# Kernel optimization log

Measured on AMD Instinct MI355X. Metric: run time of the kernel, lower is better.

The kernel has to match this reference:

```python
import jax, jax.numpy as jnp
import numpy as np

N, E, Z, C, B, G, T = 10000, 160000, 10, 64, 8, 16, 2
R_MAX = 5.0
AVG_NEIGH = 16.0
L_SLICES = ((0, 1), (1, 4), (4, 9))  # l=0,1,2 blocks of the 9 SH components


def sph_harm(u):
    # component-normalized real spherical harmonics up to l=2, u: [E,3] unit vectors
    x, y, z = u[:, 0], u[:, 1], u[:, 2]
    s3, s5, s15 = 3.0 ** 0.5, 5.0 ** 0.5, 15.0 ** 0.5
    return jnp.stack([
        jnp.ones_like(x),
        s3 * x, s3 * y, s3 * z,
        s15 * x * y, s15 * y * z, (s5 / 2) * (3 * z * z - 1), s15 * x * z, (s15 / 2) * (x * x - y * y),
    ], axis=1)  # [E,9]


def radial_embed(r):
    # Bessel basis * polynomial cutoff (p=5), r: [E]
    u = r / R_MAX
    n = jnp.arange(1, B + 1, dtype=jnp.float32)
    bessel = jnp.sqrt(2.0 / R_MAX) * jnp.sin(n[None, :] * jnp.pi * u[:, None]) / (r[:, None] + 1e-9)
    p = 5.0
    fc = 1 - (p + 1) * (p + 2) / 2 * u ** p + p * (p + 2) * u ** (p + 1) - p * (p + 1) / 2 * u ** (p + 2)
    fc = jnp.where(u < 1.0, fc, 0.0)
    return bessel * fc[:, None]  # [E,B]


def per_l_linear(x, W):
    # x: [n,C,9], W: [3,C,C]; independent channel mixing per l-block
    return jnp.concatenate([
        jnp.einsum('ncm,cd->ndm', x[:, :, s:e], W[l]) for l, (s, e) in enumerate(L_SLICES)
    ], axis=2)


def _forward(positions, node_attrs, charges, shifts, W_emb, atomic_energies,
             W_r1, W_r2, W_mix, W_sc, w_poly, W_prod, w_e, w_d,
             edge_index, batch, num_graphs):
    sender, receiver = edge_index[0], edge_index[1]
    # atomic reference energies
    node_e0 = node_attrs @ atomic_energies  # [N]
    e0 = jax.ops.segment_sum(node_e0, batch, num_segments=num_graphs)
    # node embedding: scalars only
    node_feats = jnp.zeros((positions.shape[0], C, 9), positions.dtype)
    node_feats = node_feats.at[:, :, 0].set(node_attrs @ W_emb)
    # edge geometry
    vec = positions[sender] - positions[receiver] + shifts  # [E,3]
    lengths = jnp.sqrt(jnp.sum(vec * vec, axis=1) + 1e-12)
    sh = sph_harm(vec / lengths[:, None])        # [E,9]
    edge_feats = radial_embed(lengths)           # [E,B]
    energies = [e0]
    dipoles = []
    for t in range(T):
        # radial MLP -> per-channel TP weights
        w = jax.nn.silu(edge_feats @ W_r1[t]) @ W_r2[t]      # [E,C]
        h_s = node_feats[sender, :, 0]                       # gather sender scalars [E,C]
        m = (w * h_s)[:, :, None] * sh[:, None, :]           # TP message [E,C,9]
        agg = jax.ops.segment_sum(m, receiver, num_segments=positions.shape[0]) / AVG_NEIGH
        msg = per_l_linear(agg, W_mix[t])
        sc = per_l_linear(node_feats, W_sc[t])               # self-connection
        # product basis (correlation 3): channel-wise scalar polynomial gate
        s0 = msg[:, :, 0]
        poly = w_poly[t, :, 0][None] + w_poly[t, :, 1][None] * s0 + w_poly[t, :, 2][None] * s0 * s0
        node_feats = per_l_linear(msg * poly[:, :, None], W_prod[t]) + sc
        # readout: 1x0e energy + 1x1o dipole
        e_n = node_feats[:, :, 0] @ w_e[t]                   # [N]
        energies.append(jax.ops.segment_sum(e_n, batch, num_segments=num_graphs))
        dipoles.append(jnp.einsum('ncm,c->nm', node_feats[:, :, 1:4], w_d[t]))  # [N,3]
    contributions = jnp.stack(energies, axis=-1)             # [G,T+1]
    total_energy = jnp.sum(contributions, axis=-1)           # [G]
    atomic_dipoles = jnp.sum(jnp.stack(dipoles, axis=-1), axis=-1)  # [N,3]
    total_dipole = jax.ops.segment_sum(atomic_dipoles, batch, num_segments=num_graphs)
    total_dipole = total_dipole + jax.ops.segment_sum(charges[:, None] * positions, batch, num_segments=num_graphs)
    return total_energy, contributions, atomic_dipoles, total_dipole


def setup_inputs():
    key = jax.random.key(0)
    ks = jax.random.split(key, 16)
    s = 0.1
    species = jax.random.randint(ks[1], (N,), 0, Z)
    return {
        'positions': jax.random.normal(ks[0], (N, 3)) * 3.0,
        'node_attrs': jax.nn.one_hot(species, Z, dtype=jnp.float32),
        'charges': jax.random.normal(ks[2], (N,)) * 0.1,
        'shifts': jnp.zeros((E, 3), jnp.float32),
        'W_emb': jax.random.normal(ks[5], (Z, C)) * s,
        'atomic_energies': jax.random.normal(ks[6], (Z,)) * s,
        'W_r1': jax.random.normal(ks[7], (T, B, 64)) * s,
        'W_r2': jax.random.normal(ks[8], (T, 64, C)) * s,
        'W_mix': jax.random.normal(ks[9], (T, 3, C, C)) * s,
        'W_sc': jax.random.normal(ks[10], (T, 3, C, C)) * s,
        'w_poly': jax.random.normal(ks[11], (T, C, 3)) * s,
        'W_prod': jax.random.normal(ks[12], (T, 3, C, C)) * s,
        'w_e': jax.random.normal(ks[13], (T, C)) * s,
        'w_d': jax.random.normal(ks[14], (T, C)) * s,
        'edge_index': jax.random.randint(ks[3], (2, E), 0, N),
        'batch': jnp.sort(jax.random.randint(ks[4], (N,), 0, G)),
        'num_graphs': G,
    }


def reference(positions, node_attrs, charges, shifts, W_emb, atomic_energies,
              W_r1, W_r2, W_mix, W_sc, w_poly, W_prod, w_e, w_d,
              edge_index, batch, num_graphs):
    args = (node_attrs, charges, shifts, W_emb, atomic_energies, W_r1, W_r2,
            W_mix, W_sc, w_poly, W_prod, w_e, w_d, edge_index, batch, num_graphs)
    total_energy, contributions, atomic_dipoles, total_dipole = _forward(positions, *args)
    forces = -jax.grad(lambda p: jnp.sum(_forward(p, *args)[0]))(positions)
    return total_energy, contributions, forces, total_dipole, atomic_dipoles
```

## Files before the change

kernel.cpp:

```cpp
#include <hip/hip_runtime.h>
#include <hip/hip_bf16.h>

#define NN 10000
#define NE 160000
#define NZ 10
#define NBES 8
#define NG 16
#define NT 2
#define NB 2048
#define NB1 2049
#define PL ((size_t)NN*64)

static constexpr float PI_F  = 3.14159265358979323846f;
static constexpr float KBES  = 0.63245553203367587f;
static constexpr float S3    = 1.73205080756887729f;

static constexpr size_t OFF_UVL  = 0;
static constexpr size_t OFF_PIN  = OFF_UVL + (size_t)NE*4;
static constexpr size_t OFF_ATT  = OFF_PIN + (size_t)NN*3;
static constexpr size_t OFF_CHG  = OFF_ATT + (size_t)NN*NZ;
static constexpr size_t OFF_SHF  = OFF_CHG + (size_t)NN;
static constexpr size_t OFF_NF0  = OFF_SHF + (size_t)NE*3;
static constexpr size_t OFF_NF1  = OFF_NF0 + PL;
static constexpr size_t OFF_MSG0 = OFF_NF1 + 4*PL;
static constexpr size_t OFF_MSG1 = OFF_MSG0 + 4*PL;
static constexpr size_t OFF_AGG  = OFF_MSG1 + 4*PL;
static constexpr size_t O_GA1    = OFF_AGG;
static constexpr size_t O_GA0    = OFF_AGG + 2*PL;
static constexpr size_t OFF_W    = OFF_AGG + 4*PL;
static constexpr size_t O_WEMB   = OFF_W;
static constexpr size_t O_AE     = O_WEMB + 640;
static constexpr size_t O_R1     = O_AE   + 16;
static constexpr size_t O_R2     = O_R1   + 1024;
static constexpr size_t O_WMIX   = O_R2   + 8192;
static constexpr size_t O_WMIXT  = O_WMIX + 24576;
static constexpr size_t O_WSC    = O_WMIXT+ 24576;
static constexpr size_t O_WSCT   = O_WSC  + 24576;
static constexpr size_t O_WPROD  = O_WSCT + 24576;
static constexpr size_t O_WPRODT = O_WPROD+ 24576;
static constexpr size_t O_WPOLY  = O_WPRODT+24576;
static constexpr size_t O_WE     = O_WPOLY+ 384;
static constexpr size_t O_WD     = O_WE   + 128;
static constexpr size_t OFF_ACC  = O_WD   + 128;
static constexpr size_t O_E0G    = OFF_ACC;
static constexpr size_t O_ETG    = O_E0G + 16;
static constexpr size_t O_TD     = O_ETG + 32;
static constexpr size_t O_ADP    = O_TD  + 48;
static constexpr size_t O_GPOS   = O_ADP + (size_t)NN*3;
static constexpr size_t ACC_FLOATS = 96 + (size_t)NN*6;
static constexpr size_t O_EN0    = O_GPOS + (size_t)NN*3;
static constexpr size_t O_EN1    = O_EN0 + NN;
static constexpr size_t O_E0N    = O_EN1 + NN;
static constexpr size_t O_FLAG   = O_E0N + NN;
static constexpr size_t O_TW     = O_FLAG + 4;
static constexpr size_t O_TQ     = O_TW + (size_t)2*NB1*64;
static constexpr size_t O_OFFR   = O_TQ + (size_t)2*NB1*64;
static constexpr size_t O_OFFS   = O_OFFR + (NN+1);
static constexpr size_t O_CURR   = O_OFFS + (NN+1);
static constexpr size_t O_CURS   = O_CURR + NN;
static constexpr size_t O_RECRAW = O_CURS + NN;
static constexpr size_t O_RECR   = (O_RECRAW + 7) & ~(size_t)7;
static constexpr size_t O_RECS   = O_RECR + (size_t)NE*8;
static constexpr size_t WS_FLOATS= O_RECS + (size_t)NE*8;

__device__ __forceinline__ float rlane(float v, int l){
  return __int_as_float(__builtin_amdgcn_readlane(__float_as_int(v), l));
}

static constexpr int LD_CNT[14] = {NN*3, NN*NZ, NN, NE*3, NZ*64, NZ, NT*NBES*64, NT*64*64,
                                   NT*3*64*64, NT*3*64*64, NT*64*3, NT*3*64*64, NT*64, NT*64};
static constexpr int LD_TOTAL = NN*3 + NN*NZ + NN + NE*3 + NZ*64 + NZ + NT*NBES*64 + NT*64*64
                              + 3*(NT*3*64*64) + NT*64*3 + 4*(NT*64) - NT*64*2;
__global__ __launch_bounds__(256) void k_load_all(
    const void* s0, const void* s1, const void* s2, const void* s3, const void* s4,
    const void* s5, const void* s6, const void* s7, const void* s8, const void* s9,
    const void* s10, const void* s11, const void* s12, const void* s13,
    float* __restrict__ ws){
  __shared__ int found;
  if (threadIdx.x == 0) found = 0;
  __syncthreads();
  const unsigned* raw = (const unsigned*)s1;
  int f = 0;
  for (int i = threadIdx.x; i < 4096; i += 256){
    unsigned w = raw[i];
    f |= (w == 0x00003F80u || w == 0x3F803F80u) ? 1 : 0;
  }
  if (f) found = 1;
  __syncthreads();
  const int isbf = found;
  if (blockIdx.x == 0 && threadIdx.x == 0) ((int*)(ws + O_FLAG))[0] = isbf;

  const void* srcs[14] = {s0,s1,s2,s3,s4,s5,s6,s7,s8,s9,s10,s11,s12,s13};
  const size_t dsts[14] = {OFF_PIN, OFF_ATT, OFF_CHG, OFF_SHF, O_WEMB, O_AE, O_R1, O_R2,
                           O_WMIX, O_WSC, O_WPOLY, O_WPROD, O_WE, O_WD};
  int i = blockIdx.x*256 + threadIdx.x;
  int seg = -1, off = i;
  #pragma unroll
  for (int j = 0; j < 14; ++j){
    if (seg < 0){
      if (off < LD_CNT[j]) seg = j;
      else off -= LD_CNT[j];
    }
  }
  if (seg < 0) return;
  float v = isbf ? __bfloat162float(((const __hip_bfloat16*)srcs[seg])[off])
                 : ((const float*)srcs[seg])[off];
  ws[dsts[seg] + off] = v;
}

__global__ void k_transpose_all(float* __restrict__ ws){
  const size_t srcs[3] = {O_WMIX, O_WSC, O_WPROD};
  const size_t dsts[3] = {O_WMIXT, O_WSCT, O_WPRODT};
  int i = blockIdx.x*256 + threadIdx.x;
  if (i >= 18*4096) return;
  int mm = i >> 12, r = (i >> 6) & 63, c = i & 63;
  int grp = mm / 6, m = mm % 6;
  ws[dsts[grp] + (size_t)m*4096 + (size_t)c*64 + r] =
      ws[srcs[grp] + (size_t)m*4096 + (size_t)r*64 + c];
}

static constexpr int GEOM_B = (NE+255)/256;
static constexpr int TAB_B  = (2*NB1+3)/4;
static constexpr int INIT_B = (NN+3)/4;
__global__ __launch_bounds__(256, 3) void k_prep(float* __restrict__ ws, const int* __restrict__ ei){
  int b = blockIdx.x;
  if (b < GEOM_B){
    int e = b*256 + threadIdx.x;
    if (e >= NE) return;
    const float* pos = ws + OFF_PIN;
    const float* shifts = ws + OFF_SHF;
    int s = ei[e], r = ei[NE + e];
    float vx = pos[s*3+0] - pos[r*3+0] + shifts[(size_t)e*3+0];
    float vy = pos[s*3+1] - pos[r*3+1] + shifts[(size_t)e*3+1];
    float vz = pos[s*3+2] - pos[r*3+2] + shifts[(size_t)e*3+2];
    float L = sqrtf(vx*vx + vy*vy + vz*vz + 1e-12f);
    float inv = 1.f / L;
    float4 uq; uq.x = vx*inv; uq.y = vy*inv; uq.z = vz*inv; uq.w = L;
    *(float4*)(ws + OFF_UVL + (size_t)e*4) = uq;
    if (L < 5.f){
      atomicAdd((int*)(ws + O_CURR) + r, 1);
      atomicAdd((int*)(ws + O_CURS) + s, 1);
    }
  } else if (b < GEOM_B + TAB_B){
    int lane = threadIdx.x & 63;
    int task = (b - GEOM_B)*4 + (threadIdx.x >> 6);
    if (task >= 2*NB1) return;
    int t = task / NB1, node = task % NB1;
    const float* R1 = ws + O_R1 + (size_t)t*512;
    const float* R2 = ws + O_R2 + (size_t)t*4096;
    float r1c[8];
    #pragma unroll
    for (int j = 0; j < 8; ++j) r1c[j] = R1[j*64 + lane];
    float L = fmaxf((float)node * (5.f/NB), 1e-6f);
    float ur = L*0.2f;
    float ef[8], dd[8];
    if (ur < 1.f){
      float u2=ur*ur, u4=u2*u2, u5=u4*ur;
      float fc = 1.f - 21.f*u5 + 35.f*u5*ur - 15.f*u5*u2;
      float omu = 1.f - ur;
      float dfc = -105.f*u4*omu*omu;
      float invr = 1.f/(L + 1e-9f);
      #pragma unroll
      for (int bb = 0; bb < 8; ++bb){
        float nb = (float)(bb+1);
        float arg = nb*PI_F*ur;
        float sn = __sinf(arg), cs = __cosf(arg);
        float bes = KBES*sn*invr;
        float dbes = KBES*(nb*PI_F*0.2f)*cs*invr - bes*invr;
        ef[bb] = bes*fc;
        dd[bb] = dbes*fc + bes*dfc*0.2f;
      }
    } else {
      #pragma unroll
      for (int bb = 0; bb < 8; ++bb){ ef[bb] = 0.f; dd[bb] = 0.f; }
    }
    float a = 0.f, tt = 0.f;
    #pragma unroll
    for (int bb = 0; bb < 8; ++bb){ a = fmaf(ef[bb], r1c[bb], a); tt = fmaf(r1c[bb], dd[bb], tt); }
    float sg = 1.f/(1.f + __expf(-a));
    float sl = a*sg;
    float q  = sg*fmaf(a, 1.f - sg, 1.f)*tt;
    float r2c[64];
    #pragma unroll
    for (int j = 0; j < 64; ++j) r2c[j] = R2[j*64 + lane];
    float W0=0.f, W1=0.f, Q0=0.f, Q1=0.f;
    #pragma unroll
    for (int j = 0; j < 64; j += 2){
      W0 = fmaf(rlane(sl, j  ), r2c[j  ], W0);
      W1 = fmaf(rlane(sl, j+1), r2c[j+1], W1);
      Q0 = fmaf(rlane(q,  j  ), r2c[j  ], Q0);
      Q1 = fmaf(rlane(q,  j+1), r2c[j+1], Q1);
    }
    size_t idx = ((size_t)t*NB1 + node)*64 + lane;
    ws[O_TW + idx] = (W0+W1)*(1.f/16.f);
    ws[O_TQ + idx] = (Q0+Q1)*(1.f/16.f);
  } else {
    int lane = threadIdx.x & 63;
    int n = (b - GEOM_B - TAB_B)*4 + (threadIdx.x >> 6);
    if (n >= NN) return;
    const float* attrs = ws + OFF_ATT;
    float acc = 0.f;
    #pragma unroll
    for (int z = 0; z < NZ; ++z) acc = fmaf(attrs[(size_t)n*NZ+z], ws[O_WEMB + z*64 + lane], acc);
    ws[OFF_NF0 + (size_t)n*64 + lane] = acc;
    if (lane == 0){
      float e = 0.f;
      #pragma unroll
      for (int z = 0; z < NZ; ++z) e = fmaf(attrs[(size_t)n*NZ+z], ws[O_AE + z], e);
      ws[O_E0N + n] = e;
    }
  }
}

__global__ __launch_bounds__(1024) void k_csr_scan(
    int* __restrict__ curr, int* __restrict__ curs,
    int* __restrict__ offr, int* __restrict__ offs_){
  __shared__ unsigned short cr[NN], cs[NN];
  __shared__ int pr[1024], ps[1024];
  int tid = threadIdx.x;
  for (int i = tid; i < NN; i += 1024){
    cr[i] = (unsigned short)curr[i];
    cs[i] = (unsigned short)curs[i];
  }
  __syncthreads();
  const int chunk = (NN + 1023)/1024;
  int lo = tid*chunk, hi = lo + chunk;
  if (hi > NN) hi = NN;
  if (lo > NN) lo = NN;
  int sr = 0, ss = 0;
  for (int i = lo; i < hi; ++i){ sr += cr[i]; ss += cs[i]; }
  pr[tid] = sr; ps[tid] = ss;
  __syncthreads();
  for (int o = 1; o < 1024; o <<= 1){
    int vr = (tid >= o) ? pr[tid-o] : 0;
    int vs = (tid >= o) ? ps[tid-o] : 0;
    __syncthreads();
    pr[tid] += vr; ps[tid] += vs;
    __syncthreads();
  }
  int runr = tid ? pr[tid-1] : 0;
  int runs = tid ? ps[tid-1] : 0;
  for (int i = lo; i < hi; ++i){
    int a = cr[i], c = cs[i];
    offr[i] = runr; curr[i] = runr; runr += a;
    offs_[i] = runs; curs[i] = runs; runs += c;
  }
  if (tid == 1023){ offr[NN] = runr; offs_[NN] = runs; }
}

__global__ void k_csr_fill(const int* __restrict__ ei, const float* __restrict__ uvl,
                           int* __restrict__ curr, int* __restrict__ curs,
                           float* __restrict__ recr, float* __restrict__ recs){
  int e = blockIdx.x*256 + threadIdx.x;
  if (e >= NE) return;
  float4 q = *(const float4*)(uvl + (size_t)e*4);
  if (q.w >= 5.f) return;
  int s = ei[e], r = ei[NE + e];
  int4 meta; meta.x = s; meta.y = r; meta.z = e; meta.w = 0;
  int pr = atomicAdd(&curr[r], 1);
  *(float4*)(recr + (size_t)pr*8) = q;
  *(int4*)(recr + (size_t)pr*8 + 4) = meta;
  int ps = atomicAdd(&curs[s], 1);
  *(float4*)(recs + (size_t)ps*8) = q;
  *(int4*)(recs + (size_t)ps*8 + 4) = meta;
}

__global__ __launch_bounds__(256) void k_agg(
    const float* __restrict__ TWt, const float* __restrict__ recr,
    const float* __restrict__ h, const int* __restrict__ offr,
    float* __restrict__ agg){
  int lane = threadIdx.x & 63;
  int wid = blockIdx.x*4 + (threadIdx.x >> 6);
  int nw  = gridDim.x*4;
  for (int n = wid; n < NN; n += nw){
    int lo = offr[n], hi = offr[n+1];
    float c0=0.f, x1=0.f, y1=0.f, z1=0.f;
    float d0=0.f, x2=0.f, y2=0.f, z2=0.f;
    int i = lo;
    for (; i+1 < hi; i += 2){
      const float4 qa = *(const float4*)(recr + (size_t)i*8);
      const int sa = __builtin_amdgcn_readfirstlane(((const int*)(recr + (size_t)i*8 + 4))[0]);
      const float4 qb = *(const float4*)(recr + (size_t)(i+1)*8);
      const int sb = __builtin_amdgcn_readfirstlane(((const int*)(recr + (size_t)(i+1)*8 + 4))[0]);
      float pa = qa.w*(NB/5.f); int ba = (int)pa; float fa = pa - (float)ba;
      float pb = qb.w*(NB/5.f); int bbq = (int)pb; float fb = pb - (float)bbq;
      const float* Ta = TWt + (size_t)ba*64 + lane;
      const float* Tb = TWt + (size_t)bbq*64 + lane;
      float ta0 = Ta[0], tb0 = Tb[0];
      float wa = fmaf(Ta[64]-ta0, fa, ta0);
      float wb = fmaf(Tb[64]-tb0, fb, tb0);
      float wha = wa * h[(size_t)sa*64 + lane];
      float whb = wb * h[(size_t)sb*64 + lane];
      c0 += wha; d0 += whb;
      x1 = fmaf(wha, qa.x, x1); x2 = fmaf(whb, qb.x, x2);
      y1 = fmaf(wha, qa.y, y1); y2 = fmaf(whb, qb.y, y2);
      z1 = fmaf(wha, qa.z, z1); z2 = fmaf(whb, qb.z, z2);
    }
    if (i < hi){
      const float4 q = *(const float4*)(recr + (size_t)i*8);
      const int sU = __builtin_amdgcn_readfirstlane(((const int*)(recr + (size_t)i*8 + 4))[0]);
      float pa = q.w*(NB/5.f); int ba = (int)pa; float fa = pa - (float)ba;
      const float* Ta = TWt + (size_t)ba*64 + lane;
      float ta0 = Ta[0];
      float wa = fmaf(Ta[64]-ta0, fa, ta0);
      float wha = wa * h[(size_t)sU*64 + lane];
      c0 += wha;
      x1 = fmaf(wha, q.x, x1);
      y1 = fmaf(wha, q.y, y1);
      z1 = fmaf(wha, q.z, z1);
    }
    size_t ob = (size_t)n*64 + lane;
    agg[ob]        = c0 + d0;
    agg[ob+PL]     = S3*(x1 + x2);
    agg[ob+2*PL]   = S3*(y1 + y2);
    agg[ob+3*PL]   = S3*(z1 + z2);
  }
}

__global__ __launch_bounds__(256, 3) void k_lin2(
    const float* __restrict__ in, const float* __restrict__ W3, float* __restrict__ out){
  int k = blockIdx.y;
  int l = (k==0) ? 0 : 1;
  const float* W = W3 + (size_t)l*4096;
  int lane = threadIdx.x & 63;
  float wcol[64];
  #pragma unroll
  for (int j = 0; j < 64; ++j) wcol[j] = W[j*64 + lane];
  int wid = blockIdx.x*4 + (threadIdx.x >> 6);
  int nw  = gridDim.x*4;
  const float* inp = in + (size_t)k*PL;
  float* outp = out + (size_t)k*PL;
  for (int n = wid; n < NN; n += nw){
    float x = inp[(size_t)n*64 + lane];
    float a0 = 0.f, a1 = 0.f, a2 = 0.f, a3 = 0.f;
    #pragma unroll
    for (int j = 0; j < 64; j += 4){
      a0 = fmaf(rlane(x, j  ), wcol[j  ], a0);
      a1 = fmaf(rlane(x, j+1), wcol[j+1], a1);
      a2 = fmaf(rlane(x, j+2), wcol[j+2], a2);
      a3 = fmaf(rlane(x, j+3), wcol[j+3], a3);
    }
    outp[(size_t)n*64 + lane] = (a0+a1) + (a2+a3);
  }
}

template<int WRITE_NF, int NF_SINGLE>
__global__ __launch_bounds__(256, 3) void k_tail(
    const float* __restrict__ nf_in, const float* __restrict__ msg,
    const float* __restrict__ Wsc, const float* __restrict__ Wprod, const float* __restrict__ wp,
    const float* __restrict__ we, const float* __restrict__ wd,
    float* __restrict__ nf_out, float* __restrict__ en, float* __restrict__ adp){
  int lane = threadIdx.x & 63;
  int k = threadIdx.x >> 6;
  int l = (k==0) ? 0 : 1;
  const bool use_sc = !(NF_SINGLE && k > 0);
  float wcs[64], wcp[64];
  #pragma unroll
  for (int j = 0; j < 64; ++j)
    wcp[j] = Wprod[(size_t)l*4096 + j*64 + lane];
  if (use_sc){
    #pragma unroll
    for (int j = 0; j < 64; ++j)
      wcs[j] = Wsc[(size_t)l*4096 + j*64 + lane];
  }
  float p0 = wp[lane*3], p1 = wp[lane*3+1], p2 = wp[lane*3+2];
  float rw = (k==0) ? we[lane] : wd[lane];
  const float* msgk = msg + (size_t)k*PL;
  const float* nfk  = nf_in + (size_t)k*PL;
  float* outk = nf_out + (size_t)k*PL;
  for (int n = blockIdx.x; n < NN; n += gridDim.x){
    size_t base = (size_t)n*64 + lane;
    float s0 = msg[base];
    float xm = (k==0) ? s0 : msgk[base];
    float xg = xm * fmaf(fmaf(p2, s0, p1), s0, p0);
    float b0=0.f, b1=0.f;
    #pragma unroll
    for (int j = 0; j < 64; j += 2){
      b0 = fmaf(rlane(xg, j  ), wcp[j  ], b0);
      b1 = fmaf(rlane(xg, j+1), wcp[j+1], b1);
    }
    float out = b0 + b1;
    if (use_sc){
      float xs = nfk[base];
      float a0=0.f, a1=0.f;
      #pragma unroll
      for (int j = 0; j < 64; j += 2){
        a0 = fmaf(rlane(xs, j  ), wcs[j  ], a0);
        a1 = fmaf(rlane(xs, j+1), wcs[j+1], a1);
      }
      out += a0 + a1;
    }
    if (WRITE_NF) outk[base] = out;
    float red = out * rw;
    #pragma unroll
    for (int o = 32; o; o >>= 1) red += __shfl_xor(red, o, 64);
    if (lane == 0){
      if (k == 0) en[n] = red;
      else        adp[n*3 + (k-1)] += red;
    }
  }
}

__global__ __launch_bounds__(256, 3) void k_gback1(
    const float* __restrict__ WPRODT1, const float* __restrict__ we1,
    const float* __restrict__ msg1, const float* __restrict__ wp,
    const float* __restrict__ WMIXT1, float* __restrict__ out){
  int lane = threadIdx.x & 63;
  float wcol[64];
  #pragma unroll
  for (int j = 0; j < 64; ++j) wcol[j] = WMIXT1[j*64 + lane];
  float g = 0.f;
  #pragma unroll
  for (int c = 0; c < 64; ++c) g = fmaf(we1[c], WPRODT1[c*64 + lane], g);
  float p0 = wp[lane*3], p1 = wp[lane*3+1], p2 = wp[lane*3+2];
  int wid = blockIdx.x*4 + (threadIdx.x >> 6);
  int nw  = gridDim.x*4;
  for (int n = wid; n < NN; n += nw){
    float s0 = msg1[(size_t)n*64 + lane];
    float poly = fmaf(fmaf(p2, s0, p1), s0, p0);
    float dp   = fmaf(2.f*p2, s0, p1);
    float gb = g*fmaf(s0, dp, poly);
    float a0=0.f, a1=0.f, a2=0.f, a3=0.f;
    #pragma unroll
    for (int j = 0; j < 64; j += 4){
      a0 = fmaf(rlane(gb, j  ), wcol[j  ], a0);
      a1 = fmaf(rlane(gb, j+1), wcol[j+1], a1);
      a2 = fmaf(rlane(gb, j+2), wcol[j+2], a2);
      a3 = fmaf(rlane(gb, j+3), wcol[j+3], a3);
    }
    out[(size_t)n*64 + lane] = (a0+a1) + (a2+a3);
  }
}

__global__ __launch_bounds__(256) void k_ghg0(float* __restrict__ ws, const int* __restrict__ offs_){
  __shared__ float wl[2*4096];
  for (int i = threadIdx.x; i < 4096; i += 256){
    wl[i]        = ws[O_WPRODT + i];
    wl[4096 + i] = ws[O_WMIXT + i];
  }
  __syncthreads();
  const int lane = threadIdx.x & 63;
  int wid = blockIdx.x*4 + (threadIdx.x >> 6);
  const int nw = gridDim.x*4;
  float gnfc = ws[O_WE + lane];
  {
    const float* WS1 = ws + O_WSCT + 12288;
    const float* we1 = ws + O_WE + 64;
    #pragma unroll
    for (int c = 0; c < 64; ++c) gnfc = fmaf(we1[c], WS1[c*64 + lane], gnfc);
  }
  const float p0 = ws[O_WPOLY + lane*3];
  const float p1 = ws[O_WPOLY + lane*3 + 1];
  const float p2 = ws[O_WPOLY + lane*3 + 2];
  const float* TW1 = ws + O_TW + (size_t)NB1*64;
  const float* recs = ws + O_RECS;
  const float* GA1 = ws + O_GA1;
  for (int n = wid; n < NN; n += nw){
    int lo = offs_[n], hi = offs_[n+1];
    float acc = 0.f, acc2 = 0.f;
    int i = lo;
    for (; i+1 < hi; i += 2){
      const float4 qa = *(const float4*)(recs + (size_t)i*8);
      const int ra = __builtin_amdgcn_readfirstlane(((const int*)(recs + (size_t)i*8 + 4))[1]);
      const float4 qb = *(const float4*)(recs + (size_t)(i+1)*8);
      const int rb = __builtin_amdgcn_readfirstlane(((const int*)(recs + (size_t)(i+1)*8 + 4))[1]);
      float pa = qa.w*(NB/5.f); int ba = (int)pa; float fa = pa - (float)ba;
      float pb = qb.w*(NB/5.f); int bbq = (int)pb; float fb = pb - (float)bbq;
      const float* Ta = TW1 + (size_t)ba*64 + lane;
      const float* Tb = TW1 + (size_t)bbq*64 + lane;
      float ta0 = Ta[0], tb0 = Tb[0];
      float wa = fmaf(Ta[64]-ta0, fa, ta0);
      float wb = fmaf(Tb[64]-tb0, fb, tb0);
      acc  = fmaf(wa, GA1[(size_t)ra*64 + lane], acc);
      acc2 = fmaf(wb, GA1[(size_t)rb*64 + lane], acc2);
    }
    if (i < hi){
      const float4 q = *(const float4*)(recs + (size_t)i*8);
      const int rU = __builtin_amdgcn_readfirstlane(((const int*)(recs + (size_t)i*8 + 4))[1]);
      float pa = q.w*(NB/5.f); int ba = (int)pa; float fa = pa - (float)ba;
      const float* Ta = TW1 + (size_t)ba*64 + lane;
      float ta0 = Ta[0];
      float wa = fmaf(Ta[64]-ta0, fa, ta0);
      acc = fmaf(wa, GA1[(size_t)rU*64 + lane], acc);
    }
    float gB = gnfc + (acc + acc2);
    float q0=0.f, q1=0.f;
    #pragma unroll
    for (int j = 0; j < 64; j += 2){
      q0 = fmaf(rlane(gB,j),   wl[j*64 + lane],     q0);
      q1 = fmaf(rlane(gB,j+1), wl[(j+1)*64 + lane], q1);
    }
    float gmp = q0 + q1;
    float s0v = ws[OFF_MSG0 + (size_t)n*64 + lane];
    float poly = fmaf(fmaf(p2, s0v, p1), s0v, p0);
    float dp   = fmaf(2.f*p2, s0v, p1);
    float gb = gmp * fmaf(s0v, dp, poly);
    float u0=0.f, u1=0.f;
    #pragma unroll
    for (int j = 0; j < 64; j += 2){
      u0 = fmaf(rlane(gb,j),   wl[4096 + j*64 + lane],     u0);
      u1 = fmaf(rlane(gb,j+1), wl[4096 + (j+1)*64 + lane], u1);
    }
    ws[O_GA0 + (size_t)n*64 + lane] = u0 + u1;
  }
}

__global__ __launch_bounds__(256) void k_bwdE2(float* __restrict__ ws, const int* __restrict__ nlive_ptr){
  const int lane = threadIdx.x & 63;
  int wid = blockIdx.x*4 + (threadIdx.x >> 6);
  const int nw = gridDim.x*4;
  const int nlive = nlive_ptr[0];
  const float* recs = ws + O_RECS;
  const float* TQ  = ws + O_TQ;
  const float* h0  = ws + OFF_NF0;
  const float* h1  = ws + OFF_NF1;
  const float* ga0 = ws + O_GA0;
  const float* ga1 = ws + O_GA1;
  float* gpos = ws + O_GPOS;
  for (int i = wid; i < nlive; i += nw){
    const float4 q = *(const float4*)(recs + (size_t)i*8);
    const int* meta = (const int*)(recs + (size_t)i*8 + 4);
    const int s = __builtin_amdgcn_readfirstlane(meta[0]);
    const int r = __builtin_amdgcn_readfirstlane(meta[1]);
    float posb = q.w*(NB/5.f);
    int bi = (int)posb;
    float fr = posb - (float)bi;
    const float* T0 = TQ + (size_t)bi*64 + lane;
    const float* T1 = T0 + (size_t)NB1*64;
    float Q0 = fmaf(T0[64]-T0[0], fr, T0[0]);
    float Q1 = fmaf(T1[64]-T1[0], fr, T1[0]);
    float rr = Q0*h0[(size_t)s*64 + lane]*ga0[(size_t)r*64 + lane]
             + Q1*h1[(size_t)s*64 + lane]*ga1[(size_t)r*64 + lane];
    #pragma unroll
    for (int o = 32; o; o >>= 1) rr += __shfl_xor(rr, o, 64);
    if (lane < 3){
      float u = (lane==0) ? q.x : ((lane==1) ? q.y : q.z);
      float v = rr*u;
      atomicAdd(&gpos[(size_t)s*3 + lane],  v);
      atomicAdd(&gpos[(size_t)r*3 + lane], -v);
    }
  }
}

__global__ void k_reduce(const float* __restrict__ e0n, const float* __restrict__ en0,
                         const float* __restrict__ en1, const float* __restrict__ adp,
                         const float* __restrict__ q, const float* __restrict__ pos,
                         const int* __restrict__ batch, float* __restrict__ e0g,
                         float* __restrict__ Etg, float* __restrict__ td){
  int n = blockIdx.x*256 + threadIdx.x;
  int lane = threadIdx.x & 63;
  bool valid = (n < NN);
  int g = valid ? batch[n] : -1;
  float v0=0.f, v1=0.f, v2=0.f, tx=0.f, ty=0.f, tz=0.f;
  if (valid){
    v0 = e0n[n]; v1 = en0[n]; v2 = en1[n];
    float qq = q[n];
    tx = adp[n*3+0] + qq*pos[n*3+0];
    ty = adp[n*3+1] + qq*pos[n*3+1];
    tz = adp[n*3+2] + qq*pos[n*3+2];
  }
  int g0 = __shfl(g, 0, 64), g63 = __shfl(g, 63, 64);
  if (g0 == g63 && g0 >= 0){
    #pragma unroll
    for (int o = 32; o; o >>= 1){
      v0 += __shfl_xor(v0, o, 64); v1 += __shfl_xor(v1, o, 64); v2 += __shfl_xor(v2, o, 64);
      tx += __shfl_xor(tx, o, 64); ty += __shfl_xor(ty, o, 64); tz += __shfl_xor(tz, o, 64);
    }
    if (lane == 0){
      atomicAdd(&e0g[g0], v0); atomicAdd(&Etg[g0], v1); atomicAdd(&Etg[16+g0], v2);
      atomicAdd(&td[g0*3+0], tx); atomicAdd(&td[g0*3+1], ty); atomicAdd(&td[g0*3+2], tz);
    }
  } else if (valid){
    atomicAdd(&e0g[g], v0); atomicAdd(&Etg[g], v1); atomicAdd(&Etg[16+g], v2);
    atomicAdd(&td[g*3+0], tx); atomicAdd(&td[g*3+1], ty); atomicAdd(&td[g*3+2], tz);
  }
}

__global__ void k_writeout(const float* __restrict__ e0g, const float* __restrict__ Etg,
                           const float* __restrict__ td, const float* __restrict__ adp,
                           const float* __restrict__ gpos, void* __restrict__ outv,
                           const int* __restrict__ flag){
  int i = blockIdx.x*256 + threadIdx.x;
  const int total = NG + NG*3 + NN*3 + NG*3 + NN*3;
  if (i >= total) return;
  float v;
  if (i < 16){
    v = e0g[i] + Etg[i] + Etg[16+i];
  } else if (i < 64){
    int j = i - 16; int g = j/3, t = j - g*3;
    v = (t == 0) ? e0g[g] : Etg[(t-1)*16 + g];
  } else if (i < 64 + NN*3){
    v = -gpos[i-64];
  } else if (i < 64 + NN*3 + 48){
    v = td[i - (64 + NN*3)];
  } else {
    v = adp[i - (64 + NN*3 + 48)];
  }
  if (flag[0]) ((__hip_bfloat16*)outv)[i] = __float2bfloat16(v);
  else         ((float*)outv)[i] = v;
}

extern "C" void kernel_launch(void* const* d_in, const int* in_sizes, int n_in,
                              void* d_out, int out_size, void* d_ws, size_t ws_size,
                              hipStream_t stream) {
  if (ws_size < WS_FLOATS*sizeof(float)) return;
  const int* ei    = (const int*)d_in[14];
  const int* batch = (const int*)d_in[15];
  float* ws = (float*)d_ws;

  int* offr  = (int*)(ws + O_OFFR);
  int* offs_ = (int*)(ws + O_OFFS);
  int* curr  = (int*)(ws + O_CURR);
  int* curs  = (int*)(ws + O_CURS);

  hipMemsetAsync(ws + OFF_ACC, 0, ACC_FLOATS*sizeof(float), stream);
  hipMemsetAsync(curr, 0, 2*NN*sizeof(int), stream);

  k_load_all<<<(LD_TOTAL+255)/256, 256, 0, stream>>>(
      d_in[0], d_in[1], d_in[2], d_in[3], d_in[4], d_in[5], d_in[6], d_in[7],
      d_in[8], d_in[9], d_in[10], d_in[11], d_in[12], d_in[13], ws);
  k_transpose_all<<<288, 256, 0, stream>>>(ws);
  k_prep<<<GEOM_B + TAB_B + INIT_B, 256, 0, stream>>>(ws, ei);
  k_csr_scan<<<1, 1024, 0, stream>>>(curr, curs, offr, offs_);
  k_csr_fill<<<(NE+255)/256, 256, 0, stream>>>(ei, ws+OFF_UVL, curr, curs,
                                               ws+O_RECR, ws+O_RECS);

  const size_t NF[2]  = {OFF_NF0, OFF_NF1};
  const size_t MSG[2] = {OFF_MSG0, OFF_MSG1};
  dim3 ling(256, 4);

  for (int t = 0; t < NT; ++t){
    k_agg<<<1024, 256, 0, stream>>>(ws+O_TW + (size_t)t*NB1*64, ws+O_RECR,
                                    ws+NF[t], offr, ws+OFF_AGG);
    k_lin2<<<ling, 256, 0, stream>>>(ws+OFF_AGG, ws+O_WMIX + (size_t)t*12288, ws+MSG[t]);
    if (t == 0){
      k_tail<1,1><<<1024, 256, 0, stream>>>(ws+NF[0], ws+MSG[0],
                                            ws+O_WSC, ws+O_WPROD,
                                            ws+O_WPOLY, ws+O_WE, ws+O_WD,
                                            ws+OFF_NF1, ws+O_EN0, ws+O_ADP);
    } else {
      k_tail<0,0><<<1024, 256, 0, stream>>>(ws+NF[1], ws+MSG[1],
                                            ws+O_WSC + 12288, ws+O_WPROD + 12288,
                                            ws+O_WPOLY + 192, ws+O_WE + 64, ws+O_WD + 64,
                                            ws+OFF_NF1, ws+O_EN1, ws+O_ADP);
    }
  }

  k_gback1<<<1024, 256, 0, stream>>>(ws+O_WPRODT+12288, ws+O_WE+64,
                                     ws+OFF_MSG1, ws+O_WPOLY+192,
                                     ws+O_WMIXT+12288, ws+O_GA1);
  k_ghg0<<<1024, 256, 0, stream>>>(ws, offs_);
  k_bwdE2<<<2048, 256, 0, stream>>>(ws, offs_ + NN);

  k_reduce<<<(NN+255)/256, 256, 0, stream>>>(ws+O_E0N, ws+O_EN0, ws+O_EN1, ws+O_ADP,
                                             ws+OFF_CHG, ws+OFF_PIN, batch,
                                             ws+O_E0G, ws+O_ETG, ws+O_TD);
  k_writeout<<<(60112+255)/256, 256, 0, stream>>>(ws+O_E0G, ws+O_ETG, ws+O_TD, ws+O_ADP,
                                                  ws+O_GPOS, d_out, (const int*)(ws+O_FLAG));
}
```

Baseline: 335.9 us.

## Fuse channel-mix linear into node tail kernel and fold small kernels into neighbors

Merges k_lin2 (per-l channel mixing) with k_tail into one k_node kernel per layer. The scalar message is shared across the four l-component warps through double-buffered shared memory, and only the scalar message is stored, which shrinks the message buffers. The weight transpose moves into extra blocks of k_prep and now covers only the needed matrices, and the per-graph reduction moves into extra blocks of k_ghg0, removing several launches and an intermediate round trip to global memory. In exchange each thread holds three 64-float weight columns, so occupancy is lower (launch bounds 2), the grid is smaller, and there is a block-wide sync per node.

```diff
diff --git a/kernel.cpp b/kernel.cpp
--- a/kernel.cpp
+++ b/kernel.cpp
@@ -23,8 +23,8 @@
 static constexpr size_t OFF_NF0  = OFF_SHF + (size_t)NE*3;
 static constexpr size_t OFF_NF1  = OFF_NF0 + PL;
 static constexpr size_t OFF_MSG0 = OFF_NF1 + 4*PL;
-static constexpr size_t OFF_MSG1 = OFF_MSG0 + 4*PL;
-static constexpr size_t OFF_AGG  = OFF_MSG1 + 4*PL;
+static constexpr size_t OFF_MSG1 = OFF_MSG0 + PL;
+static constexpr size_t OFF_AGG  = OFF_MSG1 + PL;
 static constexpr size_t O_GA1    = OFF_AGG;
 static constexpr size_t O_GA0    = OFF_AGG + 2*PL;
 static constexpr size_t OFF_W    = OFF_AGG + 4*PL;
@@ -108,20 +108,10 @@
   ws[dsts[seg] + off] = v;
 }
 
-__global__ void k_transpose_all(float* __restrict__ ws){
-  const size_t srcs[3] = {O_WMIX, O_WSC, O_WPROD};
-  const size_t dsts[3] = {O_WMIXT, O_WSCT, O_WPRODT};
-  int i = blockIdx.x*256 + threadIdx.x;
-  if (i >= 18*4096) return;
-  int mm = i >> 12, r = (i >> 6) & 63, c = i & 63;
-  int grp = mm / 6, m = mm % 6;
-  ws[dsts[grp] + (size_t)m*4096 + (size_t)c*64 + r] =
-      ws[srcs[grp] + (size_t)m*4096 + (size_t)r*64 + c];
-}
-
 static constexpr int GEOM_B = (NE+255)/256;
 static constexpr int TAB_B  = (2*NB1+3)/4;
 static constexpr int INIT_B = (NN+3)/4;
+static constexpr int TRAN_B = 5*4096/256;
 __global__ __launch_bounds__(256, 3) void k_prep(float* __restrict__ ws, const int* __restrict__ ei){
   int b = blockIdx.x;
   if (b < GEOM_B){
@@ -194,7 +184,7 @@
     size_t idx = ((size_t)t*NB1 + node)*64 + lane;
     ws[O_TW + idx] = (W0+W1)*(1.f/16.f);
     ws[O_TQ + idx] = (Q0+Q1)*(1.f/16.f);
-  } else {
+  } else if (b < GEOM_B + TAB_B + INIT_B){
     int lane = threadIdx.x & 63;
     int n = (b - GEOM_B - TAB_B)*4 + (threadIdx.x >> 6);
     if (n >= NN) return;
@@ -209,6 +199,12 @@
       for (int z = 0; z < NZ; ++z) e = fmaf(attrs[(size_t)n*NZ+z], ws[O_AE + z], e);
       ws[O_E0N + n] = e;
     }
+  } else {
+    int i = (b - GEOM_B - TAB_B - INIT_B)*256 + threadIdx.x;
+    int mat = i >> 12, r = (i >> 6) & 63, c = i & 63;
+    const size_t src[5] = {O_WMIX, O_WMIX+12288, O_WPROD, O_WPROD+12288, O_WSC+12288};
+    const size_t dst[5] = {O_WMIXT, O_WMIXT+12288, O_WPRODT, O_WPRODT+12288, O_WSCT+12288};
+    ws[dst[mat] + (size_t)c*64 + r] = ws[src[mat] + (size_t)r*64 + c];
   }
 }
 
@@ -317,62 +313,53 @@
   }
 }
 
-__global__ __launch_bounds__(256, 3) void k_lin2(
-    const float* __restrict__ in, const float* __restrict__ W3, float* __restrict__ out){
-  int k = blockIdx.y;
-  int l = (k==0) ? 0 : 1;
-  const float* W = W3 + (size_t)l*4096;
-  int lane = threadIdx.x & 63;
-  float wcol[64];
+static constexpr int NODE_GRID = 512;
+template<int TI>
+__global__ __launch_bounds__(256, 2) void k_node(float* __restrict__ ws){
+  __shared__ float s0buf[2][64];
+  const int lane = threadIdx.x & 63;
+  const int k = threadIdx.x >> 6;
+  const int l = (k==0) ? 0 : 1;
+  const float* Wm = ws + O_WMIX  + TI*12288 + (size_t)l*4096;
+  const float* Wp = ws + O_WPROD + TI*12288 + (size_t)l*4096;
+  const float* Wsc= ws + O_WSC   + TI*12288 + (size_t)l*4096;
+  const bool use_sc = (TI==1) || (k==0);
+  float wcm[64], wcp[64], wcs[64];
   #pragma unroll
-  for (int j = 0; j < 64; ++j) wcol[j] = W[j*64 + lane];
-  int wid = blockIdx.x*4 + (threadIdx.x >> 6);
-  int nw  = gridDim.x*4;
-  const float* inp = in + (size_t)k*PL;
-  float* outp = out + (size_t)k*PL;
-  for (int n = wid; n < NN; n += nw){
-    float x = inp[(size_t)n*64 + lane];
-    float a0 = 0.f, a1 = 0.f, a2 = 0.f, a3 = 0.f;
+  for (int j = 0; j < 64; ++j) wcm[j] = Wm[j*64 + lane];
+  #pragma unroll
+  for (int j = 0; j < 64; ++j) wcp[j] = Wp[j*64 + lane];
+  if (use_sc){
+    #pragma unroll
+    for (int j = 0; j < 64; ++j) wcs[j] = Wsc[j*64 + lane];
+  }
+  const float p0 = ws[O_WPOLY + TI*192 + lane*3];
+  const float p1 = ws[O_WPOLY + TI*192 + lane*3 + 1];
+  const float p2 = ws[O_WPOLY + TI*192 + lane*3 + 2];
+  const float rw = (k==0) ? ws[O_WE + TI*64 + lane] : ws[O_WD + TI*64 + lane];
+  const float* aggk = ws + OFF_AGG + (size_t)k*PL;
+  const float* nfk  = (TI==0) ? (ws + OFF_NF0) : (ws + OFF_NF1 + (size_t)k*PL);
+  float* msgp = ws + (TI==0 ? OFF_MSG0 : OFF_MSG1);
+  float* nfo  = ws + OFF_NF1 + (size_t)k*PL;
+  float* en   = ws + (TI==0 ? O_EN0 : O_EN1);
+  float* adp  = ws + O_ADP;
+  int it = 0;
+  for (int n = blockIdx.x; n < NN; n += NODE_GRID, ++it){
+    size_t base = (size_t)n*64 + lane;
+    float a = aggk[base];
+    float m0=0.f, m1=0.f, m2=0.f, m3=0.f;
     #pragma unroll
     for (int j = 0; j < 64; j += 4){
-      a0 = fmaf(rlane(x, j  ), wcol[j  ], a0);
-      a1 = fmaf(rlane(x, j+1), wcol[j+1], a1);
-      a2 = fmaf(rlane(x, j+2), wcol[j+2], a2);
-      a3 = fmaf(rlane(x, j+3), wcol[j+3], a3);
-    }
-    outp[(size_t)n*64 + lane] = (a0+a1) + (a2+a3);
-  }
-}
-
-template<int WRITE_NF, int NF_SINGLE>
-__global__ __launch_bounds__(256, 3) void k_tail(
-    const float* __restrict__ nf_in, const float* __restrict__ msg,
-    const float* __restrict__ Wsc, const float* __restrict__ Wprod, const float* __restrict__ wp,
-    const float* __restrict__ we, const float* __restrict__ wd,
-    float* __restrict__ nf_out, float* __restrict__ en, float* __restrict__ adp){
-  int lane = threadIdx.x & 63;
-  int k = threadIdx.x >> 6;
-  int l = (k==0) ? 0 : 1;
-  const bool use_sc = !(NF_SINGLE && k > 0);
-  float wcs[64], wcp[64];
-  #pragma unroll
-  for (int j = 0; j < 64; ++j)
-    wcp[j] = Wprod[(size_t)l*4096 + j*64 + lane];
-  if (use_sc){
-    #pragma unroll
-    for (int j = 0; j < 64; ++j)
-      wcs[j] = Wsc[(size_t)l*4096 + j*64 + lane];
-  }
-  float p0 = wp[lane*3], p1 = wp[lane*3+1], p2 = wp[lane*3+2];
-  float rw = (k==0) ? we[lane] : wd[lane];
-  const float* msgk = msg + (size_t)k*PL;
-  const float* nfk  = nf_in + (size_t)k*PL;
-  float* outk = nf_out + (size_t)k*PL;
-  for (int n = blockIdx.x; n < NN; n += gridDim.x){
-    size_t base = (size_t)n*64 + lane;
-    float s0 = msg[base];
-    float xm = (k==0) ? s0 : msgk[base];
-    float xg = xm * fmaf(fmaf(p2, s0, p1), s0, p0);
+      m0 = fmaf(rlane(a, j  ), wcm[j  ], m0);
+      m1 = fmaf(rlane(a, j+1), wcm[j+1], m1);
+      m2 = fmaf(rlane(a, j+2), wcm[j+2], m2);
+      m3 = fmaf(rlane(a, j+3), wcm[j+3], m3);
+    }
+    float m = (m0+m1) + (m2+m3);
+    if (k == 0) s0buf[it & 1][lane] = m;
+    __syncthreads();
+    float s0 = s0buf[it & 1][lane];
+    float xg = m * fmaf(fmaf(p2, s0, p1), s0, p0);
     float b0=0.f, b1=0.f;
     #pragma unroll
     for (int j = 0; j < 64; j += 2){
@@ -390,7 +377,8 @@
       }
       out += a0 + a1;
     }
-    if (WRITE_NF) outk[base] = out;
+    if (TI == 0) nfo[base] = out;
+    if (k == 0) msgp[base] = s0;
     float red = out * rw;
     #pragma unroll
     for (int o = 32; o; o >>= 1) red += __shfl_xor(red, o, 64);
@@ -432,8 +420,42 @@
   }
 }
 
-__global__ __launch_bounds__(256) void k_ghg0(float* __restrict__ ws, const int* __restrict__ offs_){
+static constexpr int GHG_GRID = 1024;
+static constexpr int RED_B = (NN+255)/256;
+__global__ __launch_bounds__(256) void k_ghg0(float* __restrict__ ws, const int* __restrict__ offs_,
+                                              const int* __restrict__ batch){
   __shared__ float wl[2*4096];
+  if (blockIdx.x >= GHG_GRID){
+    int n = (blockIdx.x - GHG_GRID)*256 + threadIdx.x;
+    int lane = threadIdx.x & 63;
+    bool valid = (n < NN);
+    int g = valid ? batch[n] : -1;
+    float v0=0.f, v1=0.f, v2=0.f, tx=0.f, ty=0.f, tz=0.f;
+    if (valid){
+      v0 = ws[O_E0N + n]; v1 = ws[O_EN0 + n]; v2 = ws[O_EN1 + n];
+      float qq = ws[OFF_CHG + n];
+      tx = ws[O_ADP + n*3+0] + qq*ws[OFF_PIN + n*3+0];
+      ty = ws[O_ADP + n*3+1] + qq*ws[OFF_PIN + n*3+1];
+      tz = ws[O_ADP + n*3+2] + qq*ws[OFF_PIN + n*3+2];
+    }
+    float* e0g = ws + O_E0G; float* Etg = ws + O_ETG; float* td = ws + O_TD;
+    int g0 = __shfl(g, 0, 64), g63 = __shfl(g, 63, 64);
+    if (g0 == g63 && g0 >= 0){
+      #pragma unroll
+      for (int o = 32; o; o >>= 1){
+        v0 += __shfl_xor(v0, o, 64); v1 += __shfl_xor(v1, o, 64); v2 += __shfl_xor(v2, o, 64);
+        tx += __shfl_xor(tx, o, 64); ty += __shfl_xor(ty, o, 64); tz += __shfl_xor(tz, o, 64);
+      }
+      if (lane == 0){
+        atomicAdd(&e0g[g0], v0); atomicAdd(&Etg[g0], v1); atomicAdd(&Etg[16+g0], v2);
+        atomicAdd(&td[g0*3+0], tx); atomicAdd(&td[g0*3+1], ty); atomicAdd(&td[g0*3+2], tz);
+      }
+    } else if (valid){
+      atomicAdd(&e0g[g], v0); atomicAdd(&Etg[g], v1); atomicAdd(&Etg[16+g], v2);
+      atomicAdd(&td[g*3+0], tx); atomicAdd(&td[g*3+1], ty); atomicAdd(&td[g*3+2], tz);
+    }
+    return;
+  }
   for (int i = threadIdx.x; i < 4096; i += 256){
     wl[i]        = ws[O_WPRODT + i];
     wl[4096 + i] = ws[O_WMIXT + i];
@@ -441,7 +463,7 @@
   __syncthreads();
   const int lane = threadIdx.x & 63;
   int wid = blockIdx.x*4 + (threadIdx.x >> 6);
-  const int nw = gridDim.x*4;
+  const int nw = GHG_GRID*4;
   float gnfc = ws[O_WE + lane];
   {
     const float* WS1 = ws + O_WSCT + 12288;
@@ -542,40 +564,6 @@
   }
 }
 
-__global__ void k_reduce(const float* __restrict__ e0n, const float* __restrict__ en0,
-                         const float* __restrict__ en1, const float* __restrict__ adp,
-                         const float* __restrict__ q, const float* __restrict__ pos,
-                         const int* __restrict__ batch, float* __restrict__ e0g,
-                         float* __restrict__ Etg, float* __restrict__ td){
-  int n = blockIdx.x*256 + threadIdx.x;
-  int lane = threadIdx.x & 63;
-  bool valid = (n < NN);
-  int g = valid ? batch[n] : -1;
-  float v0=0.f, v1=0.f, v2=0.f, tx=0.f, ty=0.f, tz=0.f;
-  if (valid){
-    v0 = e0n[n]; v1 = en0[n]; v2 = en1[n];
-    float qq = q[n];
-    tx = adp[n*3+0] + qq*pos[n*3+0];
-    ty = adp[n*3+1] + qq*pos[n*3+1];
-    tz = adp[n*3+2] + qq*pos[n*3+2];
-  }
-  int g0 = __shfl(g, 0, 64), g63 = __shfl(g, 63, 64);
-  if (g0 == g63 && g0 >= 0){
-    #pragma unroll
-    for (int o = 32; o; o >>= 1){
-      v0 += __shfl_xor(v0, o, 64); v1 += __shfl_xor(v1, o, 64); v2 += __shfl_xor(v2, o, 64);
-      tx += __shfl_xor(tx, o, 64); ty += __shfl_xor(ty, o, 64); tz += __shfl_xor(tz, o, 64);
-    }
-    if (lane == 0){
-      atomicAdd(&e0g[g0], v0); atomicAdd(&Etg[g0], v1); atomicAdd(&Etg[16+g0], v2);
-      atomicAdd(&td[g0*3+0], tx); atomicAdd(&td[g0*3+1], ty); atomicAdd(&td[g0*3+2], tz);
-    }
-  } else if (valid){
-    atomicAdd(&e0g[g], v0); atomicAdd(&Etg[g], v1); atomicAdd(&Etg[16+g], v2);
-    atomicAdd(&td[g*3+0], tx); atomicAdd(&td[g*3+1], ty); atomicAdd(&td[g*3+2], tz);
-  }
-}
-
 __global__ void k_writeout(const float* __restrict__ e0g, const float* __restrict__ Etg,
                            const float* __restrict__ td, const float* __restrict__ adp,
                            const float* __restrict__ gpos, void* __restrict__ outv,
@@ -619,42 +607,22 @@
   k_load_all<<<(LD_TOTAL+255)/256, 256, 0, stream>>>(
       d_in[0], d_in[1], d_in[2], d_in[3], d_in[4], d_in[5], d_in[6], d_in[7],
       d_in[8], d_in[9], d_in[10], d_in[11], d_in[12], d_in[13], ws);
-  k_transpose_all<<<288, 256, 0, stream>>>(ws);
-  k_prep<<<GEOM_B + TAB_B + INIT_B, 256, 0, stream>>>(ws, ei);
+  k_prep<<<GEOM_B + TAB_B + INIT_B + TRAN_B, 256, 0, stream>>>(ws, ei);
   k_csr_scan<<<1, 1024, 0, stream>>>(curr, curs, offr, offs_);
   k_csr_fill<<<(NE+255)/256, 256, 0, stream>>>(ei, ws+OFF_UVL, curr, curs,
                                                ws+O_RECR, ws+O_RECS);
 
-  const size_t NF[2]  = {OFF_NF0, OFF_NF1};
-  const size_t MSG[2] = {OFF_MSG0, OFF_MSG1};
-  dim3 ling(256, 4);
-
-  for (int t = 0; t < NT; ++t){
-    k_agg<<<1024, 256, 0, stream>>>(ws+O_TW + (size_t)t*NB1*64, ws+O_RECR,
-                                    ws+NF[t], offr, ws+OFF_AGG);
-    k_lin2<<<ling, 256, 0, stream>>>(ws+OFF_AGG, ws+O_WMIX + (size_t)t*12288, ws+MSG[t]);
-    if (t == 0){
-      k_tail<1,1><<<1024, 256, 0, stream>>>(ws+NF[0], ws+MSG[0],
-                                            ws+O_WSC, ws+O_WPROD,
-                                            ws+O_WPOLY, ws+O_WE, ws+O_WD,
-                                            ws+OFF_NF1, ws+O_EN0, ws+O_ADP);
-    } else {
-      k_tail<0,0><<<1024, 256, 0, stream>>>(ws+NF[1], ws+MSG[1],
-                                            ws+O_WSC + 12288, ws+O_WPROD + 12288,
-                                            ws+O_WPOLY + 192, ws+O_WE + 64, ws+O_WD + 64,
-                                            ws+OFF_NF1, ws+O_EN1, ws+O_ADP);
-    }
-  }
+  k_agg<<<1024, 256, 0, stream>>>(ws+O_TW, ws+O_RECR, ws+OFF_NF0, offr, ws+OFF_AGG);
+  k_node<0><<<NODE_GRID, 256, 0, stream>>>(ws);
+  k_agg<<<1024, 256, 0, stream>>>(ws+O_TW + (size_t)NB1*64, ws+O_RECR, ws+OFF_NF1, offr, ws+OFF_AGG);
+  k_node<1><<<NODE_GRID, 256, 0, stream>>>(ws);
 
   k_gback1<<<1024, 256, 0, stream>>>(ws+O_WPRODT+12288, ws+O_WE+64,
                                      ws+OFF_MSG1, ws+O_WPOLY+192,
                                      ws+O_WMIXT+12288, ws+O_GA1);
-  k_ghg0<<<1024, 256, 0, stream>>>(ws, offs_);
+  k_ghg0<<<GHG_GRID + RED_B, 256, 0, stream>>>(ws, offs_, batch);
   k_bwdE2<<<2048, 256, 0, stream>>>(ws, offs_ + NN);
 
-  k_reduce<<<(NN+255)/256, 256, 0, stream>>>(ws+O_E0N, ws+O_EN0, ws+O_EN1, ws+O_ADP,
-                                             ws+OFF_CHG, ws+OFF_PIN, batch,
-                                             ws+O_E0G, ws+O_ETG, ws+O_TD);
   k_writeout<<<(60112+255)/256, 256, 0, stream>>>(ws+O_E0G, ws+O_ETG, ws+O_TD, ws+O_ADP,
                                                   ws+O_GPOS, d_out, (const int*)(ws+O_FLAG));
 }
```

Result: slower. 345.6 us (+2.9%).
